# Performance work log

Measured on AMD Instinct MI355X. Metric: run time of the kernel, lower is better.

Reference implementation:

```python
import jax, jax.numpy as jnp
import numpy as np


def setup_inputs() -> dict:
    key = jax.random.key(0)
    k_tok, k_lp = jax.random.split(key)
    R, S, V = 512, 1024, 50257  # rows = bsz*beam, seq_len, vocab
    tokens = jax.random.randint(k_tok, (R, S), 0, V, dtype=jnp.int64)
    lprobs = jax.random.normal(k_lp, (R, V), dtype=jnp.float32)
    return {
        "tokens": tokens,
        "lprobs": lprobs,
        "bsz": 128,
        "step": 1020,
        "beam_size": 4,
        "no_repeat_ngram_size": 3,
    }


def reference(tokens, lprobs, bsz, step, beam_size, no_repeat_ngram_size):
    # Semantics of fairseq's ngram_repeat_block CUDA kernel:
    # for each row, if tokens[row, i:i+n-1] == tokens[row, step-n+2:step+1]
    # for any window start i in [0, step-n+1], ban token tokens[row, i+n-1].
    n = no_repeat_ngram_size
    R = tokens.shape[0]
    V = lprobs.shape[1]
    num_windows = step - n + 2  # static Python int

    last = tokens[:, step - n + 2 : step + 1]            # (R, n-1) final (n-1)-gram
    starts = jnp.arange(num_windows)
    win_idx = starts[:, None] + jnp.arange(n - 1)[None, :]  # (W, n-1)
    prefixes = tokens[:, win_idx]                        # (R, W, n-1)
    match = jnp.all(prefixes == last[:, None, :], axis=-1)  # (R, W) bool
    banned = tokens[:, starts + (n - 1)]                 # (R, W) tokens to ban

    # Scatter -inf into matched banned positions; unmatched windows point
    # out-of-range (index V) and are dropped.
    scatter_idx = jnp.where(match, banned, V)            # (R, W)
    rows = jnp.arange(R)[:, None]
    return lprobs.at[rows, scatter_idx].set(-jnp.inf, mode="drop")
```

## Files before the change

kernel.cpp:

```cpp
#include <hip/hip_runtime.h>
#include <math.h>

__global__ void __launch_bounds__(1024)
ngram_fused_kernel(const int* __restrict__ tokens,
                   const float* __restrict__ lprobs,
                   float* __restrict__ out,
                   const int* __restrict__ bsz_p,
                   const int* __restrict__ step_p,
                   const int* __restrict__ beam_p,
                   const int* __restrict__ n_p,
                   long long tok_elems, long long lp_elems) {
    const int bsz  = *bsz_p;
    const int step = *step_p;
    const int beam = *beam_p;
    const int n    = *n_p;

    const int R = bsz * beam;
    const long long S = tok_elems / R;
    const long long V = lp_elems / R;

    const int tid = threadIdx.x;
    const int nt  = blockDim.x;

    for (int r = blockIdx.x; r < R; r += gridDim.x) {
        const long long base = (long long)r * V;
        const long long end  = base + V;
        const long long a    = (base + 3) & ~3LL;
        const long long b    = end & ~3LL;

        for (long long i = base + tid; i < a; i += nt) out[i] = lprobs[i];
        {
            const float4* __restrict__ in4  = (const float4*)(lprobs + a);
            float4* __restrict__       out4 = (float4*)(out + a);
            const long long nv = (b - a) >> 2;
            #pragma unroll 4
            for (long long i = tid; i < nv; i += nt) out4[i] = in4[i];
        }
        for (long long i = b + tid; i < end; i += nt) out[i] = lprobs[i];

        __syncthreads();

        const int num_windows = step - n + 2;
        const int last_start  = step - n + 2;
        const int L = n - 1;
        const int* __restrict__ trow = tokens + (long long)r * S;
        for (int j = tid; j < num_windows; j += nt) {
            bool m = true;
            #pragma unroll 4
            for (int k = 0; k < L; ++k) m &= (trow[j + k] == trow[last_start + k]);
            if (m) {
                const int banned = trow[j + n - 1];
                out[base + banned] = -INFINITY;
            }
        }
        __syncthreads();
    }
}

extern "C" void kernel_launch(void* const* d_in, const int* in_sizes, int n_in,
                              void* d_out, int out_size, void* d_ws, size_t ws_size,
                              hipStream_t stream) {
    const int*   tokens = (const int*)d_in[0];
    const float* lprobs = (const float*)d_in[1];
    const int*   bsz_p  = (const int*)d_in[2];
    const int*   step_p = (const int*)d_in[3];
    const int*   beam_p = (const int*)d_in[4];
    const int*   n_p    = (const int*)d_in[5];
    float* out = (float*)d_out;

    const int blocks = 512;
    const int block  = 1024;
    ngram_fused_kernel<<<blocks, block, 0, stream>>>(
        tokens, lprobs, out, bsz_p, step_p, beam_p, n_p,
        (long long)in_sizes[0], (long long)in_sizes[1]);
}
```

Baseline: 200.8 us.

## Split each row's copy and ban pass into per-chunk blocks across a large grid

Instead of one 1024-thread block per row copying 50K floats and then scanning windows, each 256-thread block now handles one 1024-float chunk of one row. It copies a single float4 per thread, then scans all n-gram windows for that row and writes -inf only where the banned position falls inside its chunk. This gives far more concurrent blocks to saturate memory bandwidth. The cost is that every chunk repeats the window scan, about 50 times per row, although those token reads should mostly hit in cache.

```diff
diff --git a/kernel.cpp b/kernel.cpp
--- a/kernel.cpp
+++ b/kernel.cpp
@@ -1,8 +1,11 @@
 #include <hip/hip_runtime.h>
 #include <math.h>
 
-__global__ void __launch_bounds__(1024)
-ngram_fused_kernel(const int* __restrict__ tokens,
+#define NT    256
+#define CH    (NT * 4)
+
+__global__ void __launch_bounds__(NT)
+ngram_fused_chunks(const int* __restrict__ tokens,
                    const float* __restrict__ lprobs,
                    float* __restrict__ out,
                    const int* __restrict__ bsz_p,
@@ -18,39 +21,51 @@
     const int R = bsz * beam;
     const long long S = tok_elems / R;
     const long long V = lp_elems / R;
+    const int cpr = (int)((V + CH - 1) / CH);
+    const long long total_chunks = (long long)R * cpr;
 
     const int tid = threadIdx.x;
-    const int nt  = blockDim.x;
 
-    for (int r = blockIdx.x; r < R; r += gridDim.x) {
+    for (long long c = blockIdx.x; c < total_chunks; c += gridDim.x) {
+        const int r = (int)(c / cpr);
+        const int s = (int)(c - (long long)r * cpr);
+
         const long long base = (long long)r * V;
-        const long long end  = base + V;
+        const long long rend = base + V;
         const long long a    = (base + 3) & ~3LL;
-        const long long b    = end & ~3LL;
+        const long long b    = rend & ~3LL;
+        const long long nv   = (b - a) >> 2;
 
-        for (long long i = base + tid; i < a; i += nt) out[i] = lprobs[i];
-        {
-            const float4* __restrict__ in4  = (const float4*)(lprobs + a);
-            float4* __restrict__       out4 = (float4*)(out + a);
-            const long long nv = (b - a) >> 2;
-            #pragma unroll 4
-            for (long long i = tid; i < nv; i += nt) out4[i] = in4[i];
+        const long long q = (long long)s * NT + tid;
+        if (q < nv) {
+            ((float4*)(out + a))[q] = ((const float4*)(lprobs + a))[q];
         }
-        for (long long i = b + tid; i < end; i += nt) out[i] = lprobs[i];
+        if (s == 0 && tid < (int)(a - base)) {
+            out[base + tid] = lprobs[base + tid];
+        }
+        if (s == cpr - 1 && tid < (int)(rend - b)) {
+            out[b + tid] = lprobs[b + tid];
+        }
 
         __syncthreads();
+
+        long long clo = (s == 0) ? base : a + (long long)s * CH;
+        long long chi = a + (long long)(s + 1) * CH;
+        if (chi > rend || s == cpr - 1) chi = rend;
 
         const int num_windows = step - n + 2;
         const int last_start  = step - n + 2;
         const int L = n - 1;
         const int* __restrict__ trow = tokens + (long long)r * S;
-        for (int j = tid; j < num_windows; j += nt) {
+
+        for (int j = tid; j < num_windows; j += NT) {
             bool m = true;
-            #pragma unroll 4
-            for (int k = 0; k < L; ++k) m &= (trow[j + k] == trow[last_start + k]);
+            for (int k = 0; k < L; ++k) {
+                m &= (trow[j + k] == trow[last_start + k]);
+            }
             if (m) {
-                const int banned = trow[j + n - 1];
-                out[base + banned] = -INFINITY;
+                const long long pos = base + trow[j + n - 1];
+                if (pos >= clo && pos < chi) out[pos] = -INFINITY;
             }
         }
         __syncthreads();
@@ -68,9 +83,8 @@
     const int*   n_p    = (const int*)d_in[5];
     float* out = (float*)d_out;
 
-    const int blocks = 512;
-    const int block  = 1024;
-    ngram_fused_kernel<<<blocks, block, 0, stream>>>(
+    const int blocks = 25600;
+    ngram_fused_chunks<<<blocks, NT, 0, stream>>>(
         tokens, lprobs, out, bsz_p, step_p, beam_p, n_p,
         (long long)in_sizes[0], (long long)in_sizes[1]);
 }
```

Measured after the change: 217.1 us. 1.08x slower.
